# Kernel optimization log

Measured on AMD Instinct MI355X. Metric: run time of the kernel, lower is better.

Reference implementation:

```python
import jax, jax.numpy as jnp
import numpy as np

HEADS = 8

def _flatten(x, s1, s2):
    # 'b c (h s1) (w s2) -> b (h w) (s1 s2 c)'
    b, c, H, W = x.shape
    h, w = H // s1, W // s2
    x = x.reshape(b, c, h, s1, w, s2).transpose(0, 2, 4, 3, 5, 1)
    return x.reshape(b, h * w, s1 * s2 * c)

def _unflatten(x, h, w, s1, s2):
    # 'b (h w) (s1 s2 c) -> b c (h s1) (w s2)'
    b, n, e = x.shape
    c = e // (s1 * s2)
    x = x.reshape(b, h, w, s1, s2, c).transpose(0, 5, 1, 3, 2, 4)
    return x.reshape(b, c, h * s1, w * s2)

def _attn(x_detail, x_context, wq, bq, wk, bk, wv, bv, wo, bo):
    E = x_detail.shape[-1]
    d = E // HEADS
    scale = d ** -0.5
    def split(t):
        b, n, _ = t.shape
        return t.reshape(b, n, HEADS, d).transpose(0, 2, 1, 3)  # b h n d
    q = split(x_context @ wq.T + bq)
    k = split(x_detail @ wk.T + bk)
    v = split(x_detail @ wv.T + bv)
    att = jax.nn.softmax(jnp.einsum('bhqd,bhkd->bhqk', q, k) * scale, axis=-1)
    out = jnp.einsum('bhqk,bhkd->bhqd', att, v)
    b, h, n, _ = out.shape
    out = out.transpose(0, 2, 1, 3).reshape(b, n, E)
    return out @ wo.T + bo

def setup_inputs() -> dict:
    key = jax.random.key(0)
    ks = iter(jax.random.split(key, 64))
    inp = {}
    xshapes = [(16, 96, 56, 56), (16, 192, 28, 28), (16, 384, 14, 14), (16, 768, 7, 7)]
    names = ['x00', 'x10', 'x20', 'x30']
    for nm, sh in zip(names, xshapes):
        inp[nm + '_detail'] = jax.random.normal(next(ks), sh, dtype=jnp.float32)
        inp[nm + '_context'] = jax.random.normal(next(ks), sh, dtype=jnp.float32)
    embs = [384, 192, 384, 768]
    for i, E in enumerate(embs):
        for p in ['q', 'k', 'v', 'o']:
            inp[f'w{p}{i}'] = jax.random.normal(next(ks), (E, E), dtype=jnp.float32) * 0.02
            inp[f'b{p}{i}'] = jnp.zeros((E,), dtype=jnp.float32)
    return inp

def reference(x00_detail, x00_context, x10_detail, x10_context,
              x20_detail, x20_context, x30_detail, x30_context,
              wq0, bq0, wk0, bk0, wv0, bv0, wo0, bo0,
              wq1, bq1, wk1, bk1, wv1, bv1, wo1, bo1,
              wq2, bq2, wk2, bk2, wv2, bv2, wo2, bo2,
              wq3, bq3, wk3, bk3, wv3, bv3, wo3, bo3):
    # scale 0: 56x56 with 2x2 patching -> 784 tokens, emb 384
    o0 = x00_detail + _unflatten(
        _attn(_flatten(x00_detail, 2, 2), _flatten(x00_context, 2, 2),
              wq0, bq0, wk0, bk0, wv0, bv0, wo0, bo0), 28, 28, 2, 2)
    # scale 1: 28x28 -> 784 tokens, emb 192
    o1 = x10_detail + _unflatten(
        _attn(_flatten(x10_detail, 1, 1), _flatten(x10_context, 1, 1),
              wq1, bq1, wk1, bk1, wv1, bv1, wo1, bo1), 28, 28, 1, 1)
    # scale 2: 14x14 -> 196 tokens, emb 384
    o2 = x20_detail + _unflatten(
        _attn(_flatten(x20_detail, 1, 1), _flatten(x20_context, 1, 1),
              wq2, bq2, wk2, bk2, wv2, bv2, wo2, bo2), 14, 14, 1, 1)
    # scale 3: 7x7 -> 49 tokens, emb 768
    o3 = x30_detail + _unflatten(
        _attn(_flatten(x30_detail, 1, 1), _flatten(x30_context, 1, 1),
              wq3, bq3, wk3, bk3, wv3, bv3, wo3, bo3), 7, 7, 1, 1)
    return (o0, o1, o2, o3)
```

## Files before the change

kernel.cpp:

```cpp
#include <hip/hip_runtime.h>
#include <hip/hip_bf16.h>
#include <cstdint>
#include <cstddef>
#include <cmath>

typedef unsigned short bf16u;
typedef float f32x4 __attribute__((ext_vector_type(4)));
typedef short frag8 __attribute__((ext_vector_type(8)));

typedef __attribute__((address_space(1))) uint32_t u32g;
typedef __attribute__((address_space(3))) uint32_t u32l;

__device__ __forceinline__ void async_cp16(const bf16u* g, bf16u* l) {
    __builtin_amdgcn_global_load_lds((u32g*)g, (u32l*)l, 16, 0, 0);
}

__device__ __forceinline__ bf16u f2bf(float f) {
    union { float f; uint32_t u; } v; v.f = f;
    uint32_t u = v.u;
    return (bf16u)((u + 0x7fffu + ((u >> 16) & 1u)) >> 16);
}

__device__ __forceinline__ uint32_t pk2bf(float a, float b) {
    __hip_bfloat162 h = __float22bfloat162_rn(make_float2(a, b));
    union { __hip_bfloat162 h; uint32_t u; } c; c.h = h; return c.u;
}

__device__ __forceinline__ int vperm(int n) {
    return (n & ~63) | ((n & 15) << 2) | ((n >> 4) & 3);
}

static constexpr int cN[4]   = {784, 784, 196, 49};
static constexpr int cE[4]   = {384, 192, 384, 768};
static constexpr int cM[4]   = {12544, 12544, 3136, 784};
static constexpr int cC[4]   = {96, 192, 384, 768};
static constexpr int cH[4]   = {56, 28, 14, 7};
static constexpr int cS[4]   = {2, 1, 1, 1};
static constexpr int cWt[4]  = {28, 28, 14, 7};

static constexpr size_t xoff[4] = {0, 4816896, 7225344, 8429568};
static constexpr size_t voff[4] = {0, 6815744, 10223616, 12320768};
static constexpr size_t woff[4] = {0, 589824, 737280, 1327104};

__device__ __constant__ float qsc[4] = {0.20823509f, 0.29448888f, 0.20823509f, 0.14724444f};

static constexpr int qStart[13] = {0,294,588,882,957,1032,1107,1149,1191,1233,1821,2409,2997};
static constexpr int oStart[5]  = {0,294,369,411,999};

static constexpr int fStart[9] = {0,4800,9600,12000,14400,15744,17088,17856,18624};
static constexpr int wCum[17]  = {0,72,144,216,288,306,324,342,360,432,504,576,648,936,1224,1512,1800};
static constexpr int fNtn[4] = {25, 25, 7, 2};
static constexpr int fNtc[4] = {3, 6, 12, 24};
static constexpr int fSp[4]  = {4, 1, 1, 1};

struct BiasP { const float* p[16]; };
struct PrepP { const float* x[8]; const float* w[16]; };
struct OunfP { const float* xd[4]; };

__global__ __launch_bounds__(256) void prep(PrepP pp, bf16u* __restrict__ Xd,
                                            bf16u* __restrict__ Xc, bf16u* __restrict__ Wb) {
    int blk = blockIdx.x, tid = threadIdx.x;
    if (blk < 18624) {
        __shared__ float tile[32][33];
        int seg = 0;
        while (seg < 7 && blk >= fStart[seg + 1]) seg++;
        int s = seg >> 1, which = seg & 1;
        int l = blk - fStart[seg];
        int ntn = fNtn[s], ntc = fNtc[s], sp = fSp[s];
        int nt = l % ntn; l /= ntn;
        int ctl = l % ntc; l /= ntc;
        int spi = l % sp; int b = l / sp;
        int sv = cS[s];
        int s1i = spi / sv, s2i = spi % sv;
        int C = cC[s], H = cH[s], Wd = cH[s], N = cN[s], E2 = cE[s], Wt = cWt[s];
        const float* x = pp.x[s * 2 + which];
        bf16u* dst = (which ? Xc : Xd) + xoff[s];
        int tx = tid & 31, ty = tid >> 5;
        int n0 = nt * 32, c0 = ctl * 32;
#pragma unroll
        for (int rr = 0; rr < 4; ++rr) {
            int c = c0 + rr * 8 + ty;
            int n = n0 + tx;
            if (n < N) {
                int hh = (n / Wt) * sv + s1i;
                int ww = (n % Wt) * sv + s2i;
                tile[rr * 8 + ty][tx] = x[((size_t)(b * C + c) * H + hh) * Wd + ww];
            }
        }
        __syncthreads();
        int ebase = (s1i * sv + s2i) * C + c0;
#pragma unroll
        for (int rr = 0; rr < 4; ++rr) {
            int n = n0 + rr * 8 + ty;
            if (n < N)
                dst[((size_t)b * N + n) * E2 + ebase + tx] = f2bf(tile[tx][rr * 8 + ty]);
        }
    } else {
        int wb = blk - 18624;
        int m2 = 0;
        while (m2 < 15 && wb >= wCum[m2 + 1]) m2++;
        int s = m2 >> 2, mi = m2 & 3;
        size_t e2 = (size_t)cE[s] * cE[s];
        size_t base = (size_t)(wb - wCum[m2]) * 2048 + tid * 8;
        const float* src = pp.w[m2];
        bf16u* dst = Wb + woff[s] + mi * e2 + base;
        float4 a = *(const float4*)(src + base);
        float4 c = *(const float4*)(src + base + 4);
        bf16u o[8] = {f2bf(a.x), f2bf(a.y), f2bf(a.z), f2bf(a.w),
                      f2bf(c.x), f2bf(c.y), f2bf(c.z), f2bf(c.w)};
        *(frag8*)dst = *(frag8*)o;
    }
}

template<int MODE, int NN, int DHt, int DHPt, int NJt>
__device__ __forceinline__ void gemm_tile128(const bf16u* __restrict__ A, const bf16u* __restrict__ W,
                                             const float* __restrict__ bias,
                                             int M, int E, int mTile, int eTile, float oscale,
                                             bf16u* __restrict__ outB,
                                             bf16u* As, bf16u* Bs) {
    int tid = threadIdx.x, wave = tid >> 6, lane = tid & 63;
    int mbase = mTile * 128, ebase = eTile * 128;
    int wm = (wave & 1) * 64, wn = (wave >> 1) * 64;
    f32x4 acc[4][4] = {};
    int srow = tid >> 2, sch = (tid & 3) * 8;
    int K = E;
    int m0 = mbase + srow;      if (m0 >= M) m0 = M - 1;
    int m1 = mbase + srow + 64; if (m1 >= M) m1 = M - 1;
    const bf16u* Ag0 = A + (size_t)m0 * K + sch;
    const bf16u* Ag1 = A + (size_t)m1 * K + sch;
    const bf16u* Wg0 = W + (size_t)(ebase + srow) * K + sch;
    const bf16u* Wg1 = W + (size_t)(ebase + srow + 64) * K + sch;
    bf16u* Asw = As + tid * 8;
    bf16u* Bsw = Bs + tid * 8;
    int la = (lane & 15) * 32 + (lane >> 4) * 8;

    for (int k0 = 0; k0 < K; k0 += 32) {
        async_cp16(Ag0 + k0, Asw);
        async_cp16(Ag1 + k0, Asw + 2048);
        async_cp16(Wg0 + k0, Bsw);
        async_cp16(Wg1 + k0, Bsw + 2048);
        __syncthreads();
        frag8 af[4], bfr[4];
#pragma unroll
        for (int i = 0; i < 4; ++i) {
            af[i]  = *(const frag8*)(As + (wm + i * 16) * 32 + la);
            bfr[i] = *(const frag8*)(Bs + (wn + i * 16) * 32 + la);
        }
#pragma unroll
        for (int i = 0; i < 4; ++i)
#pragma unroll
            for (int j = 0; j < 4; ++j)
                acc[i][j] = __builtin_amdgcn_mfma_f32_16x16x32_bf16(af[i], bfr[j], acc[i][j], 0, 0, 0);
        __syncthreads();
    }

#pragma unroll
    for (int mt = 0; mt < 4; ++mt) {
#pragma unroll
        for (int nt = 0; nt < 4; ++nt) {
            int col = ebase + wn + nt * 16 + (lane & 15);
            float bv = bias[col];
            int rbase = mbase + wm + mt * 16 + (lane >> 4) * 4;
#pragma unroll
            for (int r = 0; r < 4; ++r) {
                int rowg = rbase + r;
                if (rowg >= M) continue;
                float val = (acc[mt][nt][r] + bv) * oscale;
                if (MODE == 0) {
                    outB[(size_t)rowg * E + col] = f2bf(val);
                } else {
                    int bb2 = rowg / NN, n = rowg % NN;
                    int hh = col / DHt, d = col - hh * DHt;
                    outB[((size_t)(bb2 * 8 + hh) * DHPt + d) * NJt + vperm(n)] = f2bf(val);
                }
            }
        }
    }
}

template<int MODE, int NN, int DHt, int DHPt, int NJt>
__device__ __forceinline__ void gemm_tile64(const bf16u* __restrict__ A, const bf16u* __restrict__ W,
                                            const float* __restrict__ bias,
                                            int M, int E, int mTile, int eTile, float oscale,
                                            bf16u* __restrict__ outB,
                                            bf16u* As, bf16u* Bs) {
    int tid = threadIdx.x, wave = tid >> 6, lane = tid & 63;
    int mbase = mTile * 64, ebase = eTile * 64;
    int wm = (wave & 1) * 32, wn = (wave >> 1) * 32;
    f32x4 acc[2][2] = {};
    int srow = tid >> 2, sch = (tid & 3) * 8;
    int K = E;
    int m = mbase + srow; if (m >= M) m = M - 1;
    const bf16u* Ag = A + (size_t)m * K + sch;
    const bf16u* Wg = W + (size_t)(ebase + srow) * K + sch;
    bf16u* Asw = As + tid * 8;
    bf16u* Bsw = Bs + tid * 8;
    int la = (lane & 15) * 32 + (lane >> 4) * 8;

    for (int k0 = 0; k0 < K; k0 += 32) {
        async_cp16(Ag + k0, Asw);
        async_cp16(Wg + k0, Bsw);
        __syncthreads();
        frag8 af0 = *(const frag8*)(As + wm * 32 + la);
        frag8 af1 = *(const frag8*)(As + (wm + 16) * 32 + la);
        frag8 bf0 = *(const frag8*)(Bs + wn * 32 + la);
        frag8 bf1 = *(const frag8*)(Bs + (wn + 16) * 32 + la);
        acc[0][0] = __builtin_amdgcn_mfma_f32_16x16x32_bf16(af0, bf0, acc[0][0], 0, 0, 0);
        acc[0][1] = __builtin_amdgcn_mfma_f32_16x16x32_bf16(af0, bf1, acc[0][1], 0, 0, 0);
        acc[1][0] = __builtin_amdgcn_mfma_f32_16x16x32_bf16(af1, bf0, acc[1][0], 0, 0, 0);
        acc[1][1] = __builtin_amdgcn_mfma_f32_16x16x32_bf16(af1, bf1, acc[1][1], 0, 0, 0);
        __syncthreads();
    }

#pragma unroll
    for (int mt = 0; mt < 2; ++mt) {
#pragma unroll
        for (int nt = 0; nt < 2; ++nt) {
            int col = ebase + wn + nt * 16 + (lane & 15);
            float bv = bias[col];
            int rbase = mbase + wm + mt * 16 + (lane >> 4) * 4;
#pragma unroll
            for (int r = 0; r < 4; ++r) {
                int rowg = rbase + r;
                if (rowg >= M) continue;
                float val = (acc[mt][nt][r] + bv) * oscale;
                if (MODE == 0) {
                    outB[(size_t)rowg * E + col] = f2bf(val);
                } else {
                    int bb2 = rowg / NN, n = rowg % NN;
                    int hh = col / DHt, d = col - hh * DHt;
                    outB[((size_t)(bb2 * 8 + hh) * DHPt + d) * NJt + vperm(n)] = f2bf(val);
                }
            }
        }
    }
}

__global__ __launch_bounds__(256) void qkv_fat(const bf16u* __restrict__ Xd, const bf16u* __restrict__ Xc,
                                               const bf16u* __restrict__ Wb,
                                               bf16u* __restrict__ Qb, bf16u* __restrict__ Kb,
                                               bf16u* __restrict__ Vt, BiasP bp) {
    __shared__ __align__(16) bf16u As[4096], Bs[4096];
    int blk = blockIdx.x;
    int seg = 0;
    while (seg < 11 && blk >= qStart[seg + 1]) seg++;
    int t = blk - qStart[seg];
    if (seg < 9) {
        int s = (seg < 3) ? 0 : (seg < 6 ? 2 : 3);
        int op = seg % 3;
        int E = cE[s], M = cM[s];
        int ct = E >> 7;
        int mTile = t / ct, eTile = t - mTile * ct;
        const bf16u* A = (op == 0 ? Xc : Xd) + xoff[s];
        const bf16u* W = Wb + woff[s] + (size_t)op * E * E;
        const float* bias = bp.p[s * 4 + op];
        if (op == 2) {
            if (s == 0)
                gemm_tile128<1, 784, 48, 64, 832>(A, W, bias, M, E, mTile, eTile, 1.0f, Vt + voff[0], As, Bs);
            else if (s == 2)
                gemm_tile128<1, 196, 48, 64, 256>(A, W, bias, M, E, mTile, eTile, 1.0f, Vt + voff[2], As, Bs);
            else
                gemm_tile128<1, 49, 96, 96, 64>(A, W, bias, M, E, mTile, eTile, 1.0f, Vt + voff[3], As, Bs);
        } else {
            float osc = (op == 0) ? qsc[s] : 1.0f;
            bf16u* outB = (op == 0 ? Qb : Kb) + xoff[s];
            gemm_tile128<0, 0, 1, 0, 0>(A, W, bias, M, E, mTile, eTile, osc, outB, As, Bs);
        }
    } else {
        int op = seg - 9;
        int E = 192, M = 12544;
        int mTile = t / 3, eTile = t - mTile * 3;
        const bf16u* A = (op == 0 ? Xc : Xd) + xoff[1];
        const bf16u* W = Wb + woff[1] + (size_t)op * E * E;
        const float* bias = bp.p[4 + op];
        if (op == 2)
            gemm_tile64<1, 784, 24, 32, 832>(A, W, bias, M, E, mTile, eTile, 1.0f, Vt + voff[1], As, Bs);
        else {
            float osc = (op == 0) ? qsc[1] : 1.0f;
            bf16u* outB = (op == 0 ? Qb : Kb) + xoff[1];
            gemm_tile64<0, 0, 1, 0, 0>(A, W, bias, M, E, mTile, eTile, osc, outB, As, Bs);
        }
    }
}

__device__ __forceinline__ f32x4 bfly_add16(f32x4 v) {
#pragma unroll
    for (int m = 1; m <= 8; m <<= 1) {
        f32x4 o;
#pragma unroll
        for (int e = 0; e < 4; ++e) o[e] = __shfl_xor(v[e], m);
#pragma unroll
        for (int e = 0; e < 4; ++e) v[e] += o[e];
    }
    return v;
}

template<int DH, int N>
__device__ __forceinline__ void attn_body2(bf16u* __restrict__ smem,
                                           const bf16u* __restrict__ Q, const bf16u* __restrict__ K,
                                           const bf16u* __restrict__ Vt, bf16u* __restrict__ O,
                                           int lin) {
    constexpr int DHP = (DH == 24) ? 32 : 64;
    constexpr int C8  = DHP / 8;
    constexpr int CM  = C8 - 1;
    constexpr int KC  = DHP / 32;
    constexpr int DHT = (DH + 15) / 16;
    constexpr int VR  = DHT * 16;
    constexpr int NT  = (N + 63) / 64;
    constexpr int NJc = NT * 64;
    constexpr int E   = DH * 8;
    constexpr int KS  = 64 * C8;
    constexpr int TS  = KS + VR * 8;
    constexpr int RND = (TS + 255) / 256;
    constexpr int PP  = 72;

    bf16u* buf0 = smem;
    bf16u* buf1 = smem + (size_t)TS * 8;
    bf16u* Ps   = smem + (size_t)2 * TS * 8;

    const int qt = lin % NT;
    const int r2 = lin / NT;
    const int h = r2 & 7, b = r2 >> 3;
    const int qb = qt * 64;
    const int tid = threadIdx.x, wave = tid >> 6, lane = tid & 63;
    const int mrow = lane & 15, quad = lane >> 4;

    const bf16u* Kb2 = K + (size_t)b * N * E + h * DH;
    const bf16u* Vb2 = Vt + (size_t)(b * 8 + h) * DHP * NJc;

    auto stage = [&](int jt, bf16u* buf) {
#pragma unroll
        for (int r = 0; r < RND; ++r) {
            int s = tid + r * 256;
            bf16u* dst = buf + (size_t)s * 8;
            if (s < KS) {
                int row = s / C8;
                int cl = (s & CM) ^ (row & CM);
                int n = jt * 64 + row; if (n >= N) n = N - 1;
                async_cp16(Kb2 + (size_t)n * E + cl * 8, dst);
            } else if (s < TS) {
                int v = s - KS;
                int d = v >> 3;
                int cl = (v & 7) ^ (d & 7);
                async_cp16(Vb2 + (size_t)d * NJc + jt * 64 + cl * 8, dst);
            }
        }
    };

    stage(0, buf0);

    frag8 qf[KC];
    {
        int qn = qb + wave * 16 + mrow; if (qn >= N) qn = N - 1;
        const bf16u* qp = Q + (size_t)(b * N + qn) * E + h * DH;
#pragma unroll
        for (int kc = 0; kc < KC; ++kc) {
            int col = kc * 32 + quad * 8;
            frag8 v = {};
            if (col < DH) v = *(const frag8*)(qp + col);
            qf[kc] = v;
        }
    }

    f32x4 lrun = {0.f, 0.f, 0.f, 0.f};
    f32x4 oacc[DHT];
#pragma unroll
    for (int t = 0; t < DHT; ++t) oacc[t] = f32x4{0.f, 0.f, 0.f, 0.f};

    bf16u* Pw = Ps + wave * 16 * PP;

    __syncthreads();

    int p = 0;
    for (int jt = 0; jt < NT; ++jt) {
        bf16u* KsB = p ? buf1 : buf0;
        bf16u* VsB = KsB + (size_t)KS * 8;
        if (jt + 1 < NT) stage(jt + 1, p ? buf0 : buf1);

        f32x4 s[4];
        const bool domask = ((N & 63) != 0) && (jt == NT - 1);
#pragma unroll
        for (int sub = 0; sub < 4; ++sub) {
            f32x4 acc = {};
#pragma unroll
            for (int kc = 0; kc < KC; ++kc) {
                int c = kc * 4 + quad;
                frag8 bfr = *(const frag8*)(KsB + ((size_t)((sub * 16 + mrow) * C8 + (c ^ (mrow & CM)))) * 8);
                acc = __builtin_amdgcn_mfma_f32_16x16x32_bf16(qf[kc], bfr, acc, 0, 0, 0);
            }
            if (domask) {
                int col = jt * 64 + sub * 16 + mrow;
                if (col >= N) { acc[0] = acc[1] = acc[2] = acc[3] = -30000.f; }
            }
            s[sub] = acc;
        }

#pragma unroll
        for (int sub = 0; sub < 4; ++sub)
#pragma unroll
            for (int e = 0; e < 4; ++e) {
                float px = __builtin_amdgcn_exp2f(s[sub][e]);
                s[sub][e] = px;
                lrun[e] += px;
            }

#pragma unroll
        for (int e = 0; e < 4; ++e) {
            uint2 u;
            u.x = pk2bf(s[0][e], s[1][e]);
            u.y = pk2bf(s[2][e], s[3][e]);
            *(uint2*)(Pw + (quad * 4 + e) * PP + mrow * 4) = u;
        }

#pragma unroll
        for (int jc = 0; jc < 2; ++jc) {
            frag8 af = *(const frag8*)(Pw + mrow * PP + jc * 32 + quad * 8);
            int c = jc * 4 + quad;
#pragma unroll
            for (int t = 0; t < DHT; ++t) {
                frag8 bfr = *(const frag8*)(VsB + ((size_t)((t * 16 + mrow) * 8 + (c ^ (mrow & 7)))) * 8);
                oacc[t] = __builtin_amdgcn_mfma_f32_16x16x32_bf16(af, bfr, oacc[t], 0, 0, 0);
            }
        }
        __syncthreads();
        p ^= 1;
    }

    lrun = bfly_add16(lrun);
    f32x4 linv;
#pragma unroll
    for (int e = 0; e < 4; ++e) linv[e] = 1.0f / lrun[e];
#pragma unroll
    for (int t = 0; t < DHT; ++t) {
        int d = t * 16 + mrow;
        if (d >= DH) continue;
#pragma unroll
        for (int e = 0; e < 4; ++e) {
            int n = qb + wave * 16 + quad * 4 + e;
            if (n < N)
                O[((size_t)(b * N + n)) * E + h * DH + d] = f2bf(oacc[t][e] * linv[e]);
        }
    }
}

__global__ __launch_bounds__(256, 4) void attn_fat(const bf16u* __restrict__ Qb, const bf16u* __restrict__ Kb,
                                                   const bf16u* __restrict__ Vt, bf16u* __restrict__ Ob) {
    __shared__ __align__(16) bf16u smem[18944];
    int blk = blockIdx.x;
    if (blk < 1664)
        attn_body2<48, 784>(smem, Qb + xoff[0], Kb + xoff[0], Vt + voff[0], Ob + xoff[0], blk);
    else if (blk < 3328)
        attn_body2<24, 784>(smem, Qb + xoff[1], Kb + xoff[1], Vt + voff[1], Ob + xoff[1], blk - 1664);
    else
        attn_body2<48, 196>(smem, Qb + xoff[2], Kb + xoff[2], Vt + voff[2], Ob + xoff[2], blk - 3328);
}

__global__ __launch_bounds__(256, 2) void attn_s3(const bf16u* __restrict__ Qg, const bf16u* __restrict__ Kg,
                                                  const bf16u* __restrict__ Vtg, bf16u* __restrict__ Og) {
    constexpr int DH = 96, N = 49, DHP = 96, KC = 3, DHT = 6, NJc = 64, E = 768;
    constexpr int KP = 104, QP = 104, VP = 72, PP = 72, C8 = 12;
    __shared__ __align__(16) bf16u smem[20224];
    bf16u* Ks = smem;
    bf16u* Vs = Ks + 64 * KP;
    bf16u* QsPw = Vs + DHT * 16 * VP;

    const bf16u* Q = Qg + xoff[3];
    const bf16u* K = Kg + xoff[3];
    const bf16u* Vt = Vtg + voff[3];
    bf16u* O = Og + xoff[3];

    int lin = blockIdx.x;
    int h = lin & 7, b = lin >> 3;
    int tid = threadIdx.x, wave = tid >> 6, lane = tid & 63;
    int mrow = lane & 15, quad = lane >> 4;

    for (int idx = tid; idx < 64 * C8; idx += 256) {
        int row = idx / C8, col = (idx % C8) * 8;
        int n = row; if (n >= N) n = N - 1;
        frag8 v = {};
        if (col < DH) v = *(const frag8*)(Q + ((size_t)(b * N + n)) * E + h * DH + col);
        *(frag8*)(QsPw + row * QP + col) = v;
    }
    for (int idx = tid; idx < 64 * C8; idx += 256) {
        int row = idx / C8, col = (idx % C8) * 8;
        int n = row; if (n >= N) n = N - 1;
        frag8 v = {};
        if (col < DH) v = *(const frag8*)(K + (size_t)(b * N + n) * E + h * DH + col);
        *(frag8*)(Ks + row * KP + col) = v;
    }
    const bf16u* Vb2 = Vt + (size_t)(b * 8 + h) * DHP * NJc;
    for (int idx = tid; idx < DHT * 16 * 8; idx += 256) {
        int d = idx / 8, j = (idx % 8) * 8;
        frag8 v = {};
        if (d < DH) v = *(const frag8*)(Vb2 + (size_t)d * NJc + j);
        *(frag8*)(Vs + d * VP + j) = v;
    }
    __syncthreads();
    frag8 qf[KC];
#pragma unroll
    for (int kc = 0; kc < KC; ++kc)
        qf[kc] = *(const frag8*)(QsPw + (wave * 16 + mrow) * QP + kc * 32 + quad * 8);
    __syncthreads();
    bf16u* Pw = QsPw + wave * 16 * PP;

    f32x4 lrun = {0.f, 0.f, 0.f, 0.f};
    f32x4 oacc[DHT];
#pragma unroll
    for (int t = 0; t < DHT; ++t) oacc[t] = f32x4{0.f, 0.f, 0.f, 0.f};

    f32x4 s[4];
#pragma unroll
    for (int sub = 0; sub < 4; ++sub) {
        f32x4 acc = {};
#pragma unroll
        for (int kc = 0; kc < KC; ++kc) {
            frag8 bfr = *(const frag8*)(Ks + (sub * 16 + mrow) * KP + kc * 32 + quad * 8);
            acc = __builtin_amdgcn_mfma_f32_16x16x32_bf16(qf[kc], bfr, acc, 0, 0, 0);
        }
        int col = sub * 16 + mrow;
        if (col >= N) { acc[0] = acc[1] = acc[2] = acc[3] = -30000.f; }
        s[sub] = acc;
    }
#pragma unroll
    for (int sub = 0; sub < 4; ++sub)
#pragma unroll
        for (int e = 0; e < 4; ++e) {
            float px = __builtin_amdgcn_exp2f(s[sub][e]);
            s[sub][e] = px;
            lrun[e] += px;
        }
#pragma unroll
    for (int e = 0; e < 4; ++e) {
        uint2 u;
        u.x = pk2bf(s[0][e], s[1][e]);
        u.y = pk2bf(s[2][e], s[3][e]);
        *(uint2*)(Pw + (quad * 4 + e) * PP + mrow * 4) = u;
    }
#pragma unroll
    for (int jc = 0; jc < 2; ++jc) {
        frag8 af = *(const frag8*)(Pw + mrow * PP + jc * 32 + quad * 8);
#pragma unroll
        for (int t = 0; t < DHT; ++t) {
            frag8 bfr = *(const frag8*)(Vs + (t * 16 + mrow) * VP + jc * 32 + quad * 8);
            oacc[t] = __builtin_amdgcn_mfma_f32_16x16x32_bf16(af, bfr, oacc[t], 0, 0, 0);
        }
    }

    lrun = bfly_add16(lrun);
    f32x4 linv;
#pragma unroll
    for (int e = 0; e < 4; ++e) linv[e] = 1.0f / lrun[e];
#pragma unroll
    for (int t = 0; t < DHT; ++t) {
        int d = t * 16 + mrow;
#pragma unroll
        for (int e = 0; e < 4; ++e) {
            int n = wave * 16 + quad * 4 + e;
            if (n < N)
                O[((size_t)(b * N + n)) * E + h * DH + d] = f2bf(oacc[t][e] * linv[e]);
        }
    }
}

template<int SC>
__device__ __forceinline__ size_t out_index(int rowg, int cg) {
    if (SC == 0) {
        int b = rowg / 784, n = rowg - b * 784;
        int slot = cg / 96, c = cg - slot * 96;
        int hh = n / 28, ww = n - hh * 28;
        return ((size_t)(b * 96 + c) * 56 + 2 * hh + (slot >> 1)) * 56 + 2 * ww + (slot & 1);
    } else if (SC == 1) {
        int b = rowg / 784, n = rowg - b * 784;
        return ((size_t)(b * 192 + cg)) * 784 + n;
    } else if (SC == 2) {
        int b = rowg / 196, n = rowg - b * 196;
        return ((size_t)(b * 384 + cg)) * 196 + n;
    } else {
        int b = rowg / 49, n = rowg - b * 49;
        return ((size_t)(b * 768 + cg)) * 49 + n;
    }
}

template<int SC>
__device__ __forceinline__ void o_tile128(const bf16u* __restrict__ A, const bf16u* __restrict__ W,
                                          const float* __restrict__ bias,
                                          const float* __restrict__ xd, float* __restrict__ out,
                                          int M, int E, int mTile, int eTile, bf16u* sm) {
    bf16u* As = sm;
    bf16u* Bs = sm + 4096;
    int tid = threadIdx.x, wave = tid >> 6, lane = tid & 63;
    int mbase = mTile * 128, ebase = eTile * 128;
    int wm = (wave & 1) * 64, wn = (wave >> 1) * 64;
    int mrow = lane & 15, quad = lane >> 4;
    f32x4 acc[4][4] = {};
    int srow = tid >> 2, sch = (tid & 3) * 8;
    int K = E;
    int m0 = mbase + srow;      if (m0 >= M) m0 = M - 1;
    int m1 = mbase + srow + 64; if (m1 >= M) m1 = M - 1;
    const bf16u* Ag0 = A + (size_t)m0 * K + sch;
    const bf16u* Ag1 = A + (size_t)m1 * K + sch;
    const bf16u* Wg0 = W + (size_t)(ebase + srow) * K + sch;
    const bf16u* Wg1 = W + (size_t)(ebase + srow + 64) * K + sch;
    bf16u* Asw = As + tid * 8;
    bf16u* Bsw = Bs + tid * 8;
    int la = mrow * 32 + quad * 8;

    for (int k0 = 0; k0 < K; k0 += 32) {
        async_cp16(Ag0 + k0, Asw);
        async_cp16(Ag1 + k0, Asw + 2048);
        async_cp16(Wg0 + k0, Bsw);
        async_cp16(Wg1 + k0, Bsw + 2048);
        __syncthreads();
        frag8 af[4], bfr[4];
#pragma unroll
        for (int i = 0; i < 4; ++i) {
            af[i]  = *(const frag8*)(As + (wm + i * 16) * 32 + la);
            bfr[i] = *(const frag8*)(Bs + (wn + i * 16) * 32 + la);
        }
#pragma unroll
        for (int i = 0; i < 4; ++i)
#pragma unroll
            for (int j = 0; j < 4; ++j)
                acc[i][j] = __builtin_amdgcn_mfma_f32_16x16x32_bf16(af[i], bfr[j], acc[i][j], 0, 0, 0);
        __syncthreads();
    }

    float* Ls = (float*)sm;
#pragma unroll
    for (int ph = 0; ph < 4; ++ph) {
        __syncthreads();
        if ((wave & 1) == (ph >> 1)) {
            int mt0 = (ph & 1) * 2;
#pragma unroll
            for (int mi = 0; mi < 2; ++mi) {
                int mt = mt0 + mi;
#pragma unroll
                for (int nt = 0; nt < 4; ++nt)
#pragma unroll
                    for (int r = 0; r < 4; ++r)
                        Ls[(mi * 16 + quad * 4 + r) * 133 + wn + nt * 16 + mrow] = acc[mt][nt][r];
            }
        }
        __syncthreads();
        int rb = mbase + ph * 32;
#pragma unroll
        for (int i = 0; i < 16; ++i) {
            int coll = (tid >> 5) + i * 8;
            int l = tid & 31;
            int rg = rb + l;
            if (rg < M) {
                int cg = ebase + coll;
                size_t oi = out_index<SC>(rg, cg);
                out[oi] = xd[oi] + Ls[l * 133 + coll] + bias[cg];
            }
        }
    }
}

__device__ __forceinline__ void o_tile64_s1(const bf16u* __restrict__ A, const bf16u* __restrict__ W,
                                            const float* __restrict__ bias,
                                            const float* __restrict__ xd, float* __restrict__ out,
                                            int M, int E, int mTile, int eTile, bf16u* sm) {
    bf16u* As = sm;
    bf16u* Bs = sm + 2048;
    int tid = threadIdx.x, wave = tid >> 6, lane = tid & 63;
    int mbase = mTile * 64, ebase = eTile * 64;
    int wm = (wave & 1) * 32, wn = (wave >> 1) * 32;
    int mrow = lane & 15, quad = lane >> 4;
    f32x4 acc[2][2] = {};
    int srow = tid >> 2, sch = (tid & 3) * 8;
    int K = E;
    int m = mbase + srow; if (m >= M) m = M - 1;
    const bf16u* Ag = A + (size_t)m * K + sch;
    const bf16u* Wg = W + (size_t)(ebase + srow) * K + sch;
    bf16u* Asw = As + tid * 8;
    bf16u* Bsw = Bs + tid * 8;
    int la = mrow * 32 + quad * 8;

    for (int k0 = 0; k0 < K; k0 += 32) {
        async_cp16(Ag + k0, Asw);
        async_cp16(Wg + k0, Bsw);
        __syncthreads();
        frag8 af0 = *(const frag8*)(As + wm * 32 + la);
        frag8 af1 = *(const frag8*)(As + (wm + 16) * 32 + la);
        frag8 bf0 = *(const frag8*)(Bs + wn * 32 + la);
        frag8 bf1 = *(const frag8*)(Bs + (wn + 16) * 32 + la);
        acc[0][0] = __builtin_amdgcn_mfma_f32_16x16x32_bf16(af0, bf0, acc[0][0], 0, 0, 0);
        acc[0][1] = __builtin_amdgcn_mfma_f32_16x16x32_bf16(af0, bf1, acc[0][1], 0, 0, 0);
        acc[1][0] = __builtin_amdgcn_mfma_f32_16x16x32_bf16(af1, bf0, acc[1][0], 0, 0, 0);
        acc[1][1] = __builtin_amdgcn_mfma_f32_16x16x32_bf16(af1, bf1, acc[1][1], 0, 0, 0);
        __syncthreads();
    }

    float* Ls = (float*)sm;
#pragma unroll
    for (int ph = 0; ph < 2; ++ph) {
        __syncthreads();
        if ((wave & 1) == ph) {
#pragma unroll
            for (int mt = 0; mt < 2; ++mt)
#pragma unroll
                for (int nt = 0; nt < 2; ++nt)
#pragma unroll
                    for (int r = 0; r < 4; ++r)
                        Ls[(mt * 16 + quad * 4 + r) * 69 + wn + nt * 16 + mrow] = acc[mt][nt][r];
        }
        __syncthreads();
        int rb = mbase + ph * 32;
#pragma unroll
        for (int i = 0; i < 8; ++i) {
            int coll = (tid >> 5) + i * 8;
            int l = tid & 31;
            int rg = rb + l;
            if (rg < M) {
                int cg = ebase + coll;
                size_t oi = out_index<1>(rg, cg);
                out[oi] = xd[oi] + Ls[l * 69 + coll] + bias[cg];
            }
        }
    }
}

__global__ __launch_bounds__(256) void ounf_fat(const bf16u* __restrict__ Ob, const bf16u* __restrict__ Wb,
                                                float* __restrict__ out, BiasP bp, OunfP up) {
    __shared__ __align__(16) bf16u sm[8512];
    int blk = blockIdx.x;
    int seg = 0;
    while (seg < 3 && blk >= oStart[seg + 1]) seg++;
    int t = blk - oStart[seg];
    if (seg < 3) {
        int s = (seg == 0) ? 0 : (seg == 1 ? 2 : 3);
        int E = cE[s], M = cM[s];
        int ct = E >> 7;
        int mTile = t / ct, eTile = t - mTile * ct;
        const bf16u* A = Ob + xoff[s];
        const bf16u* W = Wb + woff[s] + (size_t)3 * E * E;
        if (s == 0)
            o_tile128<0>(A, W, bp.p[3], up.xd[0], out + xoff[0], M, E, mTile, eTile, sm);
        else if (s == 2)
            o_tile128<2>(A, W, bp.p[11], up.xd[2], out + xoff[2], M, E, mTile, eTile, sm);
        else
            o_tile128<3>(A, W, bp.p[15], up.xd[3], out + xoff[3], M, E, mTile, eTile, sm);
    } else {
        int E = 192, M = 12544;
        int mTile = t / 3, eTile = t - mTile * 3;
        o_tile64_s1(Ob + xoff[1], Wb + woff[1] + (size_t)3 * E * E, bp.p[7],
                    up.xd[1], out + xoff[1], M, E, mTile, eTile, sm);
    }
}

extern "C" void kernel_launch(void* const* d_in, const int* in_sizes, int n_in,
                              void* d_out, int out_size, void* d_ws, size_t ws_size,
                              hipStream_t stream) {
    bf16u* ws = (bf16u*)d_ws;
    bf16u* Qb = ws;
    bf16u* Kb = ws + 9031680;
    bf16u* Vt = ws + 18063360;
    bf16u* Ob = ws + 31170560;
    bf16u* Wb = ws + 40202240;
    bf16u* Xd = ws + 43888640;
    bf16u* Xc = ws + 52920320;
    float* out = (float*)d_out;

    PrepP pp; BiasP bb; OunfP ux;
    for (int s = 0; s < 4; ++s) {
        pp.x[s * 2]     = (const float*)d_in[s * 2];
        pp.x[s * 2 + 1] = (const float*)d_in[s * 2 + 1];
        ux.xd[s]        = (const float*)d_in[s * 2];
        int w0 = 8 + s * 8;
        pp.w[s * 4 + 0] = (const float*)d_in[w0 + 0];
        pp.w[s * 4 + 1] = (const float*)d_in[w0 + 2];
        pp.w[s * 4 + 2] = (const float*)d_in[w0 + 4];
        pp.w[s * 4 + 3] = (const float*)d_in[w0 + 6];
        bb.p[s * 4 + 0] = (const float*)d_in[w0 + 1];
        bb.p[s * 4 + 1] = (const float*)d_in[w0 + 3];
        bb.p[s * 4 + 2] = (const float*)d_in[w0 + 5];
        bb.p[s * 4 + 3] = (const float*)d_in[w0 + 7];
    }

    prep<<<20424, 256, 0, stream>>>(pp, Xd, Xc, Wb);
    qkv_fat<<<2997, 256, 0, stream>>>(Xd, Xc, Wb, Qb, Kb, Vt, bb);
    attn_fat<<<3840, 256, 0, stream>>>(Qb, Kb, Vt, Ob);
    attn_s3<<<128, 256, 0, stream>>>(Qb, Kb, Vt, Ob);
    ounf_fat<<<999, 256, 0, stream>>>(Ob, Wb, out, bb, ux);
}
```

Before: 382.0 us.

## Double-buffer LDS staging in QKV and output projection GEMM tiles

Gives the 128- and 64-wide GEMM tiles in both the QKV and output-projection kernels two LDS buffers. The async global-to-LDS copy for the next K-slice is issued before the MFMAs on the current slice run, and the barriers per K step drop from two to one. The aim is to hide global load latency behind matrix math. In exchange, shared memory per block roughly doubles, which can lower the number of resident blocks per CU.

```diff
diff --git a/kernel.cpp b/kernel.cpp
--- a/kernel.cpp
+++ b/kernel.cpp
@@ -117,7 +117,7 @@
                                              const float* __restrict__ bias,
                                              int M, int E, int mTile, int eTile, float oscale,
                                              bf16u* __restrict__ outB,
-                                             bf16u* As, bf16u* Bs) {
+                                             bf16u* sm) {
     int tid = threadIdx.x, wave = tid >> 6, lane = tid & 63;
     int mbase = mTile * 128, ebase = eTile * 128;
     int wm = (wave & 1) * 64, wn = (wave >> 1) * 64;
@@ -130,28 +130,38 @@
     const bf16u* Ag1 = A + (size_t)m1 * K + sch;
     const bf16u* Wg0 = W + (size_t)(ebase + srow) * K + sch;
     const bf16u* Wg1 = W + (size_t)(ebase + srow + 64) * K + sch;
-    bf16u* Asw = As + tid * 8;
-    bf16u* Bsw = Bs + tid * 8;
     int la = (lane & 15) * 32 + (lane >> 4) * 8;
 
-    for (int k0 = 0; k0 < K; k0 += 32) {
+    auto stage = [&](int k0, bf16u* buf) {
+        bf16u* Asw = buf + tid * 8;
+        bf16u* Bsw = buf + 4096 + tid * 8;
         async_cp16(Ag0 + k0, Asw);
         async_cp16(Ag1 + k0, Asw + 2048);
         async_cp16(Wg0 + k0, Bsw);
         async_cp16(Wg1 + k0, Bsw + 2048);
-        __syncthreads();
+    };
+
+    stage(0, sm);
+    __syncthreads();
+    int cur = 0;
+    for (int k0 = 0; k0 < K; k0 += 32) {
+        bf16u* buf = sm + cur * 8192;
+        bool more = (k0 + 32 < K);
+        if (more) stage(k0 + 32, sm + (cur ^ 1) * 8192);
+        const bf16u* AsB = buf;
+        const bf16u* BsB = buf + 4096;
         frag8 af[4], bfr[4];
 #pragma unroll
         for (int i = 0; i < 4; ++i) {
-            af[i]  = *(const frag8*)(As + (wm + i * 16) * 32 + la);
-            bfr[i] = *(const frag8*)(Bs + (wn + i * 16) * 32 + la);
+            af[i]  = *(const frag8*)(AsB + (wm + i * 16) * 32 + la);
+            bfr[i] = *(const frag8*)(BsB + (wn + i * 16) * 32 + la);
         }
 #pragma unroll
         for (int i = 0; i < 4; ++i)
 #pragma unroll
             for (int j = 0; j < 4; ++j)
                 acc[i][j] = __builtin_amdgcn_mfma_f32_16x16x32_bf16(af[i], bfr[j], acc[i][j], 0, 0, 0);
-        __syncthreads();
+        if (more) { __syncthreads(); cur ^= 1; }
     }
 
 #pragma unroll
@@ -183,7 +193,7 @@
                                             const float* __restrict__ bias,
                                             int M, int E, int mTile, int eTile, float oscale,
                                             bf16u* __restrict__ outB,
-                                            bf16u* As, bf16u* Bs) {
+                                            bf16u* sm) {
     int tid = threadIdx.x, wave = tid >> 6, lane = tid & 63;
     int mbase = mTile * 64, ebase = eTile * 64;
     int wm = (wave & 1) * 32, wn = (wave >> 1) * 32;
@@ -193,23 +203,29 @@
     int m = mbase + srow; if (m >= M) m = M - 1;
     const bf16u* Ag = A + (size_t)m * K + sch;
     const bf16u* Wg = W + (size_t)(ebase + srow) * K + sch;
-    bf16u* Asw = As + tid * 8;
-    bf16u* Bsw = Bs + tid * 8;
     int la = (lane & 15) * 32 + (lane >> 4) * 8;
 
+    auto stage = [&](int k0, bf16u* buf) {
+        async_cp16(Ag + k0, buf + tid * 8);
+        async_cp16(Wg + k0, buf + 2048 + tid * 8);
+    };
+
+    stage(0, sm);
+    __syncthreads();
+    int cur = 0;
     for (int k0 = 0; k0 < K; k0 += 32) {
-        async_cp16(Ag + k0, Asw);
-        async_cp16(Wg + k0, Bsw);
-        __syncthreads();
-        frag8 af0 = *(const frag8*)(As + wm * 32 + la);
-        frag8 af1 = *(const frag8*)(As + (wm + 16) * 32 + la);
-        frag8 bf0 = *(const frag8*)(Bs + wn * 32 + la);
-        frag8 bf1 = *(const frag8*)(Bs + (wn + 16) * 32 + la);
+        bf16u* buf = sm + cur * 4096;
+        bool more = (k0 + 32 < K);
+        if (more) stage(k0 + 32, sm + (cur ^ 1) * 4096);
+        frag8 af0 = *(const frag8*)(buf + wm * 32 + la);
+        frag8 af1 = *(const frag8*)(buf + (wm + 16) * 32 + la);
+        frag8 bf0 = *(const frag8*)(buf + 2048 + wn * 32 + la);
+        frag8 bf1 = *(const frag8*)(buf + 2048 + (wn + 16) * 32 + la);
         acc[0][0] = __builtin_amdgcn_mfma_f32_16x16x32_bf16(af0, bf0, acc[0][0], 0, 0, 0);
         acc[0][1] = __builtin_amdgcn_mfma_f32_16x16x32_bf16(af0, bf1, acc[0][1], 0, 0, 0);
         acc[1][0] = __builtin_amdgcn_mfma_f32_16x16x32_bf16(af1, bf0, acc[1][0], 0, 0, 0);
         acc[1][1] = __builtin_amdgcn_mfma_f32_16x16x32_bf16(af1, bf1, acc[1][1], 0, 0, 0);
-        __syncthreads();
+        if (more) { __syncthreads(); cur ^= 1; }
     }
 
 #pragma unroll
@@ -240,7 +256,7 @@
                                                const bf16u* __restrict__ Wb,
                                                bf16u* __restrict__ Qb, bf16u* __restrict__ Kb,
                                                bf16u* __restrict__ Vt, BiasP bp) {
-    __shared__ __align__(16) bf16u As[4096], Bs[4096];
+    __shared__ __align__(16) bf16u sm[16384];
     int blk = blockIdx.x;
     int seg = 0;
     while (seg < 11 && blk >= qStart[seg + 1]) seg++;
@@ -256,15 +272,15 @@
         const float* bias = bp.p[s * 4 + op];
         if (op == 2) {
             if (s == 0)
-                gemm_tile128<1, 784, 48, 64, 832>(A, W, bias, M, E, mTile, eTile, 1.0f, Vt + voff[0], As, Bs);
+                gemm_tile128<1, 784, 48, 64, 832>(A, W, bias, M, E, mTile, eTile, 1.0f, Vt + voff[0], sm);
             else if (s == 2)
-                gemm_tile128<1, 196, 48, 64, 256>(A, W, bias, M, E, mTile, eTile, 1.0f, Vt + voff[2], As, Bs);
+                gemm_tile128<1, 196, 48, 64, 256>(A, W, bias, M, E, mTile, eTile, 1.0f, Vt + voff[2], sm);
             else
-                gemm_tile128<1, 49, 96, 96, 64>(A, W, bias, M, E, mTile, eTile, 1.0f, Vt + voff[3], As, Bs);
+                gemm_tile128<1, 49, 96, 96, 64>(A, W, bias, M, E, mTile, eTile, 1.0f, Vt + voff[3], sm);
         } else {
             float osc = (op == 0) ? qsc[s] : 1.0f;
             bf16u* outB = (op == 0 ? Qb : Kb) + xoff[s];
-            gemm_tile128<0, 0, 1, 0, 0>(A, W, bias, M, E, mTile, eTile, osc, outB, As, Bs);
+            gemm_tile128<0, 0, 1, 0, 0>(A, W, bias, M, E, mTile, eTile, osc, outB, sm);
         }
     } else {
         int op = seg - 9;
@@ -274,11 +290,11 @@
         const bf16u* W = Wb + woff[1] + (size_t)op * E * E;
         const float* bias = bp.p[4 + op];
         if (op == 2)
-            gemm_tile64<1, 784, 24, 32, 832>(A, W, bias, M, E, mTile, eTile, 1.0f, Vt + voff[1], As, Bs);
+            gemm_tile64<1, 784, 24, 32, 832>(A, W, bias, M, E, mTile, eTile, 1.0f, Vt + voff[1], sm);
         else {
             float osc = (op == 0) ? qsc[1] : 1.0f;
             bf16u* outB = (op == 0 ? Qb : Kb) + xoff[1];
-            gemm_tile64<0, 0, 1, 0, 0>(A, W, bias, M, E, mTile, eTile, osc, outB, As, Bs);
+            gemm_tile64<0, 0, 1, 0, 0>(A, W, bias, M, E, mTile, eTile, osc, outB, sm);
         }
     }
 }
@@ -586,8 +602,6 @@
                                           const float* __restrict__ bias,
                                           const float* __restrict__ xd, float* __restrict__ out,
                                           int M, int E, int mTile, int eTile, bf16u* sm) {
-    bf16u* As = sm;
-    bf16u* Bs = sm + 4096;
     int tid = threadIdx.x, wave = tid >> 6, lane = tid & 63;
     int mbase = mTile * 128, ebase = eTile * 128;
     int wm = (wave & 1) * 64, wn = (wave >> 1) * 64;
@@ -601,28 +615,38 @@
     const bf16u* Ag1 = A + (size_t)m1 * K + sch;
     const bf16u* Wg0 = W + (size_t)(ebase + srow) * K + sch;
     const bf16u* Wg1 = W + (size_t)(ebase + srow + 64) * K + sch;
-    bf16u* Asw = As + tid * 8;
-    bf16u* Bsw = Bs + tid * 8;
     int la = mrow * 32 + quad * 8;
 
-    for (int k0 = 0; k0 < K; k0 += 32) {
+    auto stage = [&](int k0, bf16u* buf) {
+        bf16u* Asw = buf + tid * 8;
+        bf16u* Bsw = buf + 4096 + tid * 8;
         async_cp16(Ag0 + k0, Asw);
         async_cp16(Ag1 + k0, Asw + 2048);
         async_cp16(Wg0 + k0, Bsw);
         async_cp16(Wg1 + k0, Bsw + 2048);
-        __syncthreads();
+    };
+
+    stage(0, sm);
+    __syncthreads();
+    int cur = 0;
+    for (int k0 = 0; k0 < K; k0 += 32) {
+        bf16u* buf = sm + cur * 8192;
+        bool more = (k0 + 32 < K);
+        if (more) stage(k0 + 32, sm + (cur ^ 1) * 8192);
+        const bf16u* AsB = buf;
+        const bf16u* BsB = buf + 4096;
         frag8 af[4], bfr[4];
 #pragma unroll
         for (int i = 0; i < 4; ++i) {
-            af[i]  = *(const frag8*)(As + (wm + i * 16) * 32 + la);
-            bfr[i] = *(const frag8*)(Bs + (wn + i * 16) * 32 + la);
+            af[i]  = *(const frag8*)(AsB + (wm + i * 16) * 32 + la);
+            bfr[i] = *(const frag8*)(BsB + (wn + i * 16) * 32 + la);
         }
 #pragma unroll
         for (int i = 0; i < 4; ++i)
 #pragma unroll
             for (int j = 0; j < 4; ++j)
                 acc[i][j] = __builtin_amdgcn_mfma_f32_16x16x32_bf16(af[i], bfr[j], acc[i][j], 0, 0, 0);
-        __syncthreads();
+        if (more) { __syncthreads(); cur ^= 1; }
     }
 
     float* Ls = (float*)sm;
@@ -661,8 +685,6 @@
                                             const float* __restrict__ bias,
                                             const float* __restrict__ xd, float* __restrict__ out,
                                             int M, int E, int mTile, int eTile, bf16u* sm) {
-    bf16u* As = sm;
-    bf16u* Bs = sm + 2048;
     int tid = threadIdx.x, wave = tid >> 6, lane = tid & 63;
     int mbase = mTile * 64, ebase = eTile * 64;
     int wm = (wave & 1) * 32, wn = (wave >> 1) * 32;
@@ -673,23 +695,29 @@
     int m = mbase + srow; if (m >= M) m = M - 1;
     const bf16u* Ag = A + (size_t)m * K + sch;
     const bf16u* Wg = W + (size_t)(ebase + srow) * K + sch;
-    bf16u* Asw = As + tid * 8;
-    bf16u* Bsw = Bs + tid * 8;
     int la = mrow * 32 + quad * 8;
 
+    auto stage = [&](int k0, bf16u* buf) {
+        async_cp16(Ag + k0, buf + tid * 8);
+        async_cp16(Wg + k0, buf + 2048 + tid * 8);
+    };
+
+    stage(0, sm);
+    __syncthreads();
+    int cur = 0;
     for (int k0 = 0; k0 < K; k0 += 32) {
-        async_cp16(Ag + k0, Asw);
-        async_cp16(Wg + k0, Bsw);
-        __syncthreads();
-        frag8 af0 = *(const frag8*)(As + wm * 32 + la);
-        frag8 af1 = *(const frag8*)(As + (wm + 16) * 32 + la);
-        frag8 bf0 = *(const frag8*)(Bs + wn * 32 + la);
-        frag8 bf1 = *(const frag8*)(Bs + (wn + 16) * 32 + la);
+        bf16u* buf = sm + cur * 4096;
+        bool more = (k0 + 32 < K);
+        if (more) stage(k0 + 32, sm + (cur ^ 1) * 4096);
+        frag8 af0 = *(const frag8*)(buf + wm * 32 + la);
+        frag8 af1 = *(const frag8*)(buf + (wm + 16) * 32 + la);
+        frag8 bf0 = *(const frag8*)(buf + 2048 + wn * 32 + la);
+        frag8 bf1 = *(const frag8*)(buf + 2048 + (wn + 16) * 32 + la);
         acc[0][0] = __builtin_amdgcn_mfma_f32_16x16x32_bf16(af0, bf0, acc[0][0], 0, 0, 0);
         acc[0][1] = __builtin_amdgcn_mfma_f32_16x16x32_bf16(af0, bf1, acc[0][1], 0, 0, 0);
         acc[1][0] = __builtin_amdgcn_mfma_f32_16x16x32_bf16(af1, bf0, acc[1][0], 0, 0, 0);
         acc[1][1] = __builtin_amdgcn_mfma_f32_16x16x32_bf16(af1, bf1, acc[1][1], 0, 0, 0);
-        __syncthreads();
+        if (more) { __syncthreads(); cur ^= 1; }
     }
 
     float* Ls = (float*)sm;
@@ -723,7 +751,7 @@
 
 __global__ __launch_bounds__(256) void ounf_fat(const bf16u* __restrict__ Ob, const bf16u* __restrict__ Wb,
                                                 float* __restrict__ out, BiasP bp, OunfP up) {
-    __shared__ __align__(16) bf16u sm[8512];
+    __shared__ __align__(16) bf16u sm[16384];
     int blk = blockIdx.x;
     int seg = 0;
     while (seg < 3 && blk >= oStart[seg + 1]) seg++;
```

New measurement: 422.8 us. 1.11x slower.

## Double-buffer LDS tiles in QKV and output-projection GEMMs

Applied to the files above, without the earlier changes.

Every 128- and 64-wide GEMM tile routine (QKV projection and output projection with unflatten) now uses two LDS buffers. The async global-to-LDS copy of the next 32-wide K slice is issued before the MFMA work on the current slice, which halves the number of barriers per K step. The aim is to hide global load latency behind matrix math. In exchange, shared memory per block doubles to 32 KB, which can lower how many blocks fit on each CU.

```diff
diff --git a/kernel.cpp b/kernel.cpp
--- a/kernel.cpp
+++ b/kernel.cpp
@@ -117,7 +117,11 @@
                                              const float* __restrict__ bias,
                                              int M, int E, int mTile, int eTile, float oscale,
                                              bf16u* __restrict__ outB,
-                                             bf16u* As, bf16u* Bs) {
+                                             bf16u* sm) {
+    bf16u* A0 = sm;
+    bf16u* B0 = sm + 4096;
+    bf16u* A1 = sm + 8192;
+    bf16u* B1 = sm + 12288;
     int tid = threadIdx.x, wave = tid >> 6, lane = tid & 63;
     int mbase = mTile * 128, ebase = eTile * 128;
     int wm = (wave & 1) * 64, wn = (wave >> 1) * 64;
@@ -130,16 +134,15 @@
     const bf16u* Ag1 = A + (size_t)m1 * K + sch;
     const bf16u* Wg0 = W + (size_t)(ebase + srow) * K + sch;
     const bf16u* Wg1 = W + (size_t)(ebase + srow + 64) * K + sch;
-    bf16u* Asw = As + tid * 8;
-    bf16u* Bsw = Bs + tid * 8;
     int la = (lane & 15) * 32 + (lane >> 4) * 8;
 
-    for (int k0 = 0; k0 < K; k0 += 32) {
-        async_cp16(Ag0 + k0, Asw);
-        async_cp16(Ag1 + k0, Asw + 2048);
-        async_cp16(Wg0 + k0, Bsw);
-        async_cp16(Wg1 + k0, Bsw + 2048);
-        __syncthreads();
+    auto stage = [&](int k0, bf16u* As, bf16u* Bs) {
+        async_cp16(Ag0 + k0, As + tid * 8);
+        async_cp16(Ag1 + k0, As + 2048 + tid * 8);
+        async_cp16(Wg0 + k0, Bs + tid * 8);
+        async_cp16(Wg1 + k0, Bs + 2048 + tid * 8);
+    };
+    auto compute = [&](const bf16u* As, const bf16u* Bs) {
         frag8 af[4], bfr[4];
 #pragma unroll
         for (int i = 0; i < 4; ++i) {
@@ -151,7 +154,17 @@
 #pragma unroll
             for (int j = 0; j < 4; ++j)
                 acc[i][j] = __builtin_amdgcn_mfma_f32_16x16x32_bf16(af[i], bfr[j], acc[i][j], 0, 0, 0);
-        __syncthreads();
+    };
+
+    stage(0, A0, B0);
+    __syncthreads();
+    for (int k0 = 0; k0 < K; k0 += 64) {
+        stage(k0 + 32, A1, B1);
+        compute(A0, B0);
+        __syncthreads();
+        if (k0 + 64 < K) stage(k0 + 64, A0, B0);
+        compute(A1, B1);
+        if (k0 + 64 < K) __syncthreads();
     }
 
 #pragma unroll
@@ -183,7 +196,11 @@
                                             const float* __restrict__ bias,
                                             int M, int E, int mTile, int eTile, float oscale,
                                             bf16u* __restrict__ outB,
-                                            bf16u* As, bf16u* Bs) {
+                                            bf16u* sm) {
+    bf16u* A0 = sm;
+    bf16u* B0 = sm + 2048;
+    bf16u* A1 = sm + 4096;
+    bf16u* B1 = sm + 6144;
     int tid = threadIdx.x, wave = tid >> 6, lane = tid & 63;
     int mbase = mTile * 64, ebase = eTile * 64;
     int wm = (wave & 1) * 32, wn = (wave >> 1) * 32;
@@ -193,14 +210,13 @@
     int m = mbase + srow; if (m >= M) m = M - 1;
     const bf16u* Ag = A + (size_t)m * K + sch;
     const bf16u* Wg = W + (size_t)(ebase + srow) * K + sch;
-    bf16u* Asw = As + tid * 8;
-    bf16u* Bsw = Bs + tid * 8;
     int la = (lane & 15) * 32 + (lane >> 4) * 8;
 
-    for (int k0 = 0; k0 < K; k0 += 32) {
-        async_cp16(Ag + k0, Asw);
-        async_cp16(Wg + k0, Bsw);
-        __syncthreads();
+    auto stage = [&](int k0, bf16u* As, bf16u* Bs) {
+        async_cp16(Ag + k0, As + tid * 8);
+        async_cp16(Wg + k0, Bs + tid * 8);
+    };
+    auto compute = [&](const bf16u* As, const bf16u* Bs) {
         frag8 af0 = *(const frag8*)(As + wm * 32 + la);
         frag8 af1 = *(const frag8*)(As + (wm + 16) * 32 + la);
         frag8 bf0 = *(const frag8*)(Bs + wn * 32 + la);
@@ -209,7 +225,17 @@
         acc[0][1] = __builtin_amdgcn_mfma_f32_16x16x32_bf16(af0, bf1, acc[0][1], 0, 0, 0);
         acc[1][0] = __builtin_amdgcn_mfma_f32_16x16x32_bf16(af1, bf0, acc[1][0], 0, 0, 0);
         acc[1][1] = __builtin_amdgcn_mfma_f32_16x16x32_bf16(af1, bf1, acc[1][1], 0, 0, 0);
-        __syncthreads();
+    };
+
+    stage(0, A0, B0);
+    __syncthreads();
+    for (int k0 = 0; k0 < K; k0 += 64) {
+        stage(k0 + 32, A1, B1);
+        compute(A0, B0);
+        __syncthreads();
+        if (k0 + 64 < K) stage(k0 + 64, A0, B0);
+        compute(A1, B1);
+        if (k0 + 64 < K) __syncthreads();
     }
 
 #pragma unroll
@@ -240,7 +266,7 @@
                                                const bf16u* __restrict__ Wb,
                                                bf16u* __restrict__ Qb, bf16u* __restrict__ Kb,
                                                bf16u* __restrict__ Vt, BiasP bp) {
-    __shared__ __align__(16) bf16u As[4096], Bs[4096];
+    __shared__ __align__(16) bf16u sm[16384];
     int blk = blockIdx.x;
     int seg = 0;
     while (seg < 11 && blk >= qStart[seg + 1]) seg++;
@@ -256,15 +282,15 @@
         const float* bias = bp.p[s * 4 + op];
         if (op == 2) {
             if (s == 0)
-                gemm_tile128<1, 784, 48, 64, 832>(A, W, bias, M, E, mTile, eTile, 1.0f, Vt + voff[0], As, Bs);
+                gemm_tile128<1, 784, 48, 64, 832>(A, W, bias, M, E, mTile, eTile, 1.0f, Vt + voff[0], sm);
             else if (s == 2)
-                gemm_tile128<1, 196, 48, 64, 256>(A, W, bias, M, E, mTile, eTile, 1.0f, Vt + voff[2], As, Bs);
+                gemm_tile128<1, 196, 48, 64, 256>(A, W, bias, M, E, mTile, eTile, 1.0f, Vt + voff[2], sm);
             else
-                gemm_tile128<1, 49, 96, 96, 64>(A, W, bias, M, E, mTile, eTile, 1.0f, Vt + voff[3], As, Bs);
+                gemm_tile128<1, 49, 96, 96, 64>(A, W, bias, M, E, mTile, eTile, 1.0f, Vt + voff[3], sm);
         } else {
             float osc = (op == 0) ? qsc[s] : 1.0f;
             bf16u* outB = (op == 0 ? Qb : Kb) + xoff[s];
-            gemm_tile128<0, 0, 1, 0, 0>(A, W, bias, M, E, mTile, eTile, osc, outB, As, Bs);
+            gemm_tile128<0, 0, 1, 0, 0>(A, W, bias, M, E, mTile, eTile, osc, outB, sm);
         }
     } else {
         int op = seg - 9;
@@ -274,11 +300,11 @@
         const bf16u* W = Wb + woff[1] + (size_t)op * E * E;
         const float* bias = bp.p[4 + op];
         if (op == 2)
-            gemm_tile64<1, 784, 24, 32, 832>(A, W, bias, M, E, mTile, eTile, 1.0f, Vt + voff[1], As, Bs);
+            gemm_tile64<1, 784, 24, 32, 832>(A, W, bias, M, E, mTile, eTile, 1.0f, Vt + voff[1], sm);
         else {
             float osc = (op == 0) ? qsc[1] : 1.0f;
             bf16u* outB = (op == 0 ? Qb : Kb) + xoff[1];
-            gemm_tile64<0, 0, 1, 0, 0>(A, W, bias, M, E, mTile, eTile, osc, outB, As, Bs);
+            gemm_tile64<0, 0, 1, 0, 0>(A, W, bias, M, E, mTile, eTile, osc, outB, sm);
         }
     }
 }
@@ -586,8 +612,10 @@
                                           const float* __restrict__ bias,
                                           const float* __restrict__ xd, float* __restrict__ out,
                                           int M, int E, int mTile, int eTile, bf16u* sm) {
-    bf16u* As = sm;
-    bf16u* Bs = sm + 4096;
+    bf16u* A0 = sm;
+    bf16u* B0 = sm + 4096;
+    bf16u* A1 = sm + 8192;
+    bf16u* B1 = sm + 12288;
     int tid = threadIdx.x, wave = tid >> 6, lane = tid & 63;
     int mbase = mTile * 128, ebase = eTile * 128;
     int wm = (wave & 1) * 64, wn = (wave >> 1) * 64;
@@ -601,16 +629,15 @@
     const bf16u* Ag1 = A + (size_t)m1 * K + sch;
     const bf16u* Wg0 = W + (size_t)(ebase + srow) * K + sch;
     const bf16u* Wg1 = W + (size_t)(ebase + srow + 64) * K + sch;
-    bf16u* Asw = As + tid * 8;
-    bf16u* Bsw = Bs + tid * 8;
     int la = mrow * 32 + quad * 8;
 
-    for (int k0 = 0; k0 < K; k0 += 32) {
-        async_cp16(Ag0 + k0, Asw);
-        async_cp16(Ag1 + k0, Asw + 2048);
-        async_cp16(Wg0 + k0, Bsw);
-        async_cp16(Wg1 + k0, Bsw + 2048);
-        __syncthreads();
+    auto stage = [&](int k0, bf16u* As, bf16u* Bs) {
+        async_cp16(Ag0 + k0, As + tid * 8);
+        async_cp16(Ag1 + k0, As + 2048 + tid * 8);
+        async_cp16(Wg0 + k0, Bs + tid * 8);
+        async_cp16(Wg1 + k0, Bs + 2048 + tid * 8);
+    };
+    auto compute = [&](const bf16u* As, const bf16u* Bs) {
         frag8 af[4], bfr[4];
 #pragma unroll
         for (int i = 0; i < 4; ++i) {
@@ -622,7 +649,17 @@
 #pragma unroll
             for (int j = 0; j < 4; ++j)
                 acc[i][j] = __builtin_amdgcn_mfma_f32_16x16x32_bf16(af[i], bfr[j], acc[i][j], 0, 0, 0);
-        __syncthreads();
+    };
+
+    stage(0, A0, B0);
+    __syncthreads();
+    for (int k0 = 0; k0 < K; k0 += 64) {
+        stage(k0 + 32, A1, B1);
+        compute(A0, B0);
+        __syncthreads();
+        if (k0 + 64 < K) stage(k0 + 64, A0, B0);
+        compute(A1, B1);
+        if (k0 + 64 < K) __syncthreads();
     }
 
     float* Ls = (float*)sm;
@@ -661,8 +698,10 @@
                                             const float* __restrict__ bias,
                                             const float* __restrict__ xd, float* __restrict__ out,
                                             int M, int E, int mTile, int eTile, bf16u* sm) {
-    bf16u* As = sm;
-    bf16u* Bs = sm + 2048;
+    bf16u* A0 = sm;
+    bf16u* B0 = sm + 2048;
+    bf16u* A1 = sm + 4096;
+    bf16u* B1 = sm + 6144;
     int tid = threadIdx.x, wave = tid >> 6, lane = tid & 63;
     int mbase = mTile * 64, ebase = eTile * 64;
     int wm = (wave & 1) * 32, wn = (wave >> 1) * 32;
@@ -673,14 +712,13 @@
     int m = mbase + srow; if (m >= M) m = M - 1;
     const bf16u* Ag = A + (size_t)m * K + sch;
     const bf16u* Wg = W + (size_t)(ebase + srow) * K + sch;
-    bf16u* Asw = As + tid * 8;
-    bf16u* Bsw = Bs + tid * 8;
     int la = mrow * 32 + quad * 8;
 
-    for (int k0 = 0; k0 < K; k0 += 32) {
-        async_cp16(Ag + k0, Asw);
-        async_cp16(Wg + k0, Bsw);
-        __syncthreads();
+    auto stage = [&](int k0, bf16u* As, bf16u* Bs) {
+        async_cp16(Ag + k0, As + tid * 8);
+        async_cp16(Wg + k0, Bs + tid * 8);
+    };
+    auto compute = [&](const bf16u* As, const bf16u* Bs) {
         frag8 af0 = *(const frag8*)(As + wm * 32 + la);
         frag8 af1 = *(const frag8*)(As + (wm + 16) * 32 + la);
         frag8 bf0 = *(const frag8*)(Bs + wn * 32 + la);
@@ -689,7 +727,17 @@
         acc[0][1] = __builtin_amdgcn_mfma_f32_16x16x32_bf16(af0, bf1, acc[0][1], 0, 0, 0);
         acc[1][0] = __builtin_amdgcn_mfma_f32_16x16x32_bf16(af1, bf0, acc[1][0], 0, 0, 0);
         acc[1][1] = __builtin_amdgcn_mfma_f32_16x16x32_bf16(af1, bf1, acc[1][1], 0, 0, 0);
-        __syncthreads();
+    };
+
+    stage(0, A0, B0);
+    __syncthreads();
+    for (int k0 = 0; k0 < K; k0 += 64) {
+        stage(k0 + 32, A1, B1);
+        compute(A0, B0);
+        __syncthreads();
+        if (k0 + 64 < K) stage(k0 + 64, A0, B0);
+        compute(A1, B1);
+        if (k0 + 64 < K) __syncthreads();
     }
 
     float* Ls = (float*)sm;
@@ -723,7 +771,7 @@
 
 __global__ __launch_bounds__(256) void ounf_fat(const bf16u* __restrict__ Ob, const bf16u* __restrict__ Wb,
                                                 float* __restrict__ out, BiasP bp, OunfP up) {
-    __shared__ __align__(16) bf16u sm[8512];
+    __shared__ __align__(16) bf16u sm[16384];
     int blk = blockIdx.x;
     int seg = 0;
     while (seg < 3 && blk >= oStart[seg + 1]) seg++;
```

Measured after the change: 375.9 us. Within noise of the previous version (-1.6%).
